# Optimization experiments

Hardware: AMD Instinct MI355X
Metric: run time of the kernel (lower is better)

Reference implementation:

```python
import jax, jax.numpy as jnp
import numpy as np

N_NODES = 40000
N_EDGES = 640000
IN_DIM, HID_DIM, OUT_DIM = 512, 128, 40


def setup_inputs() -> dict:
    key = jax.random.key(0)
    ks = jax.random.split(key, 8)
    x = jax.random.normal(ks[0], (N_NODES, IN_DIM), dtype=jnp.float32)
    edge_row = jax.random.randint(ks[1], (N_EDGES,), 0, N_NODES, dtype=jnp.int32)
    edge_col = jax.random.randint(ks[2], (N_EDGES,), 0, N_NODES, dtype=jnp.int32)
    edge_val = jax.random.uniform(ks[3], (N_EDGES,), dtype=jnp.float32)
    # Xavier-uniform init like nn.init.xavier_uniform_
    lim1 = float(np.sqrt(6.0 / (IN_DIM + HID_DIM)))
    lim2 = float(np.sqrt(6.0 / (HID_DIM + OUT_DIM)))
    W1 = jax.random.uniform(ks[4], (IN_DIM, HID_DIM), minval=-lim1, maxval=lim1, dtype=jnp.float32)
    W2 = jax.random.uniform(ks[5], (HID_DIM, OUT_DIM), minval=-lim2, maxval=lim2, dtype=jnp.float32)
    b1 = jnp.zeros((HID_DIM,), dtype=jnp.float32)
    b2 = jnp.zeros((OUT_DIM,), dtype=jnp.float32)
    return {"x": x, "edge_row": edge_row, "edge_col": edge_col, "edge_val": edge_val,
            "W1": W1, "b1": b1, "W2": W2, "b2": b2}


def _spmm(edge_row, edge_col, edge_val, y):
    # sparse adj @ y : gather source-node rows, scale by edge weight, scatter-add to dest
    msgs = edge_val[:, None] * y[edge_col]            # [E, d]
    return jax.ops.segment_sum(msgs, edge_row, num_segments=N_NODES)  # [N, d]


def reference(x, edge_row, edge_col, edge_val, W1, b1, W2, b2):
    # layer 1: dense projection + SpMM + bias
    h = _spmm(edge_row, edge_col, edge_val, x @ W1) + b1   # [N, hid]
    h = jax.nn.relu(h)
    # dropout is identity in eval mode (reference runs in eval)
    # layer 2
    o = _spmm(edge_row, edge_col, edge_val, h @ W2) + b2   # [N, out]
    return jax.nn.log_softmax(o, axis=1)
```

## Files before the change

kernel.cpp:

```cpp
#include <hip/hip_runtime.h>
#include <hip/hip_bf16.h>
#include <math.h>

#define N_NODES 40000
#define N_EDGES 640000
#define IN_DIM 512
#define HID_DIM 128
#define OUT_DIM 40
#define W2_PAD 48
#define SEG 64

typedef __attribute__((ext_vector_type(8))) short bf16x8_t;
typedef __attribute__((ext_vector_type(4))) float f32x4_t;

static __device__ __forceinline__ unsigned short f2bf(float f) {
    unsigned u = __float_as_uint(f);
    u += 0x7FFFu + ((u >> 16) & 1u);
    return (unsigned short)(u >> 16);
}
static __device__ __forceinline__ float bflo(unsigned g) { return __uint_as_float(g << 16); }
static __device__ __forceinline__ float bfhi(unsigned g) { return __uint_as_float(g & 0xFFFF0000u); }

__global__ __launch_bounds__(256) void convert_zero_kernel(const float* __restrict__ W1,
                                                           const float* __restrict__ W2,
                                                           unsigned short* __restrict__ w1t,
                                                           unsigned short* __restrict__ w2t,
                                                           int* __restrict__ cursor) {
    int idx = blockIdx.x * 256 + threadIdx.x;
    if (idx < N_NODES / 4) {
        reinterpret_cast<int4*>(cursor)[idx] = make_int4(0, 0, 0, 0);
    }
    if (idx < IN_DIM * HID_DIM) {
        int k = idx >> 7;
        int n = idx & 127;
        w1t[n * IN_DIM + k] = f2bf(W1[idx]);
    } else if (idx < IN_DIM * HID_DIM + W2_PAD * HID_DIM) {
        int j = idx - IN_DIM * HID_DIM;
        int n = j >> 7;
        int k = j & 127;
        w2t[n * HID_DIM + k] = (n < OUT_DIM) ? f2bf(W2[k * OUT_DIM + n]) : 0;
    }
}

__global__ __launch_bounds__(256) void scatter_kernel(const int* __restrict__ erow,
                                                      const int* __restrict__ ecol,
                                                      const float* __restrict__ eval,
                                                      int* __restrict__ cursor,
                                                      unsigned* __restrict__ sortedP) {
    int e = blockIdx.x * 256 + threadIdx.x;
    if (e < N_EDGES) {
        int r = erow[e];
        int pos = atomicAdd(&cursor[r], 1);
        sortedP[r * SEG + pos] = (unsigned)ecol[e] | ((unsigned)f2bf(eval[e]) << 16);
    }
}

__global__ __launch_bounds__(256) void gemm1_mfma_kernel(const float* __restrict__ x,
                                                         const unsigned short* __restrict__ w1t,
                                                         unsigned short* __restrict__ y1b) {
    __shared__ unsigned short Al[64][40];
    __shared__ unsigned short Bl[128][40];
    const int t    = threadIdx.x;
    const int wave = t >> 6;
    const int lane = t & 63;
    const int m0   = blockIdx.x * 64;
    const int mrow = lane & 15;
    const int quad = lane >> 4;

    const int ar = t >> 2;
    const int ac = (t & 3) * 8;
    const float* xptr = &x[(size_t)(m0 + ar) * IN_DIM + ac];
    const unsigned short* bptr0 = &w1t[(size_t)(t >> 2) * IN_DIM + (t & 3) * 8];
    const unsigned short* bptr1 = bptr0 + (size_t)64 * IN_DIM;

    f32x4_t acc[8];
#pragma unroll
    for (int i = 0; i < 8; ++i) acc[i] = (f32x4_t){0.f, 0.f, 0.f, 0.f};

    float4 xa = *reinterpret_cast<const float4*>(xptr);
    float4 xb = *reinterpret_cast<const float4*>(xptr + 4);
    int4   bw0 = *reinterpret_cast<const int4*>(bptr0);
    int4   bw1 = *reinterpret_cast<const int4*>(bptr1);

    for (int k0 = 0; k0 < IN_DIM; k0 += 32) {
        {
            union { int4 v; __hip_bfloat162 b[4]; } pk;
            pk.b[0] = __float22bfloat162_rn(make_float2(xa.x, xa.y));
            pk.b[1] = __float22bfloat162_rn(make_float2(xa.z, xa.w));
            pk.b[2] = __float22bfloat162_rn(make_float2(xb.x, xb.y));
            pk.b[3] = __float22bfloat162_rn(make_float2(xb.z, xb.w));
            *reinterpret_cast<int4*>(&Al[ar][ac]) = pk.v;
            *reinterpret_cast<int4*>(&Bl[t >> 2][(t & 3) * 8]) = bw0;
            *reinterpret_cast<int4*>(&Bl[64 + (t >> 2)][(t & 3) * 8]) = bw1;
        }
        __syncthreads();

        if (k0 + 32 < IN_DIM) {
            xa  = *reinterpret_cast<const float4*>(xptr + k0 + 32);
            xb  = *reinterpret_cast<const float4*>(xptr + k0 + 36);
            bw0 = *reinterpret_cast<const int4*>(bptr0 + k0 + 32);
            bw1 = *reinterpret_cast<const int4*>(bptr1 + k0 + 32);
        }

        bf16x8_t a = *reinterpret_cast<const bf16x8_t*>(&Al[wave * 16 + mrow][quad * 8]);
#pragma unroll
        for (int nt = 0; nt < 8; ++nt) {
            bf16x8_t b = *reinterpret_cast<const bf16x8_t*>(&Bl[nt * 16 + mrow][quad * 8]);
            acc[nt] = __builtin_amdgcn_mfma_f32_16x16x32_bf16(a, b, acc[nt], 0, 0, 0);
        }
        __syncthreads();
    }

#pragma unroll
    for (int nt = 0; nt < 8; ++nt) {
#pragma unroll
        for (int reg = 0; reg < 4; ++reg) {
            int row = m0 + wave * 16 + quad * 4 + reg;
            y1b[(size_t)row * HID_DIM + nt * 16 + mrow] = f2bf(acc[nt][reg]);
        }
    }
}

__global__ __launch_bounds__(256) void spmm1_kernel(const int* __restrict__ counts,
                                                    const unsigned* __restrict__ sortedP,
                                                    const unsigned short* __restrict__ y1b,
                                                    const float* __restrict__ b1,
                                                    unsigned short* __restrict__ h_bf) {
    const int lane = threadIdx.x & 63;
    const int q    = lane >> 4;
    const int fl   = lane & 15;
    const int row  = blockIdx.x * 4 + (threadIdx.x >> 6);
    const int cnt  = counts[row];
    unsigned meta  = (lane < cnt) ? sortedP[row * SEG + lane] : 0u;
    float a[8] = {0.f, 0.f, 0.f, 0.f, 0.f, 0.f, 0.f, 0.f};

    for (int j = 0; j < cnt; j += 8) {
        unsigned p0 = (unsigned)__shfl((int)meta, j + q, 64);
        unsigned p1 = (unsigned)__shfl((int)meta, j + 4 + q, 64);
        float v0 = __uint_as_float(p0 & 0xFFFF0000u);
        float v1 = __uint_as_float(p1 & 0xFFFF0000u);
        int   c0 = p0 & 0xFFFF;
        int   c1 = p1 & 0xFFFF;
        uint4 g0 = *reinterpret_cast<const uint4*>(&y1b[(size_t)c0 * HID_DIM + fl * 8]);
        uint4 g1 = *reinterpret_cast<const uint4*>(&y1b[(size_t)c1 * HID_DIM + fl * 8]);
        a[0] += v0 * bflo(g0.x); a[1] += v0 * bfhi(g0.x);
        a[2] += v0 * bflo(g0.y); a[3] += v0 * bfhi(g0.y);
        a[4] += v0 * bflo(g0.z); a[5] += v0 * bfhi(g0.z);
        a[6] += v0 * bflo(g0.w); a[7] += v0 * bfhi(g0.w);
        a[0] += v1 * bflo(g1.x); a[1] += v1 * bfhi(g1.x);
        a[2] += v1 * bflo(g1.y); a[3] += v1 * bfhi(g1.y);
        a[4] += v1 * bflo(g1.z); a[5] += v1 * bfhi(g1.z);
        a[6] += v1 * bflo(g1.w); a[7] += v1 * bfhi(g1.w);
    }
#pragma unroll
    for (int i = 0; i < 8; ++i) {
        a[i] += __shfl_xor(a[i], 16, 64);
        a[i] += __shfl_xor(a[i], 32, 64);
    }
    if (q == 0) {
        float4 vb0 = *reinterpret_cast<const float4*>(&b1[fl * 8]);
        float4 vb1 = *reinterpret_cast<const float4*>(&b1[fl * 8 + 4]);
        union { uint4 v; __hip_bfloat162 b[4]; } pk;
        pk.b[0] = __float22bfloat162_rn(make_float2(fmaxf(a[0] + vb0.x, 0.f), fmaxf(a[1] + vb0.y, 0.f)));
        pk.b[1] = __float22bfloat162_rn(make_float2(fmaxf(a[2] + vb0.z, 0.f), fmaxf(a[3] + vb0.w, 0.f)));
        pk.b[2] = __float22bfloat162_rn(make_float2(fmaxf(a[4] + vb1.x, 0.f), fmaxf(a[5] + vb1.y, 0.f)));
        pk.b[3] = __float22bfloat162_rn(make_float2(fmaxf(a[6] + vb1.z, 0.f), fmaxf(a[7] + vb1.w, 0.f)));
        *reinterpret_cast<uint4*>(&h_bf[(size_t)row * HID_DIM + fl * 8]) = pk.v;
    }
}

__global__ __launch_bounds__(256) void gemm2_mfma_kernel(const unsigned short* __restrict__ h_bf,
                                                         const unsigned short* __restrict__ w2t,
                                                         unsigned short* __restrict__ y2) {
    __shared__ unsigned short Hs[64][136];
    __shared__ unsigned short Ws[W2_PAD][136];
    const int t    = threadIdx.x;
    const int wave = t >> 6;
    const int lane = t & 63;
    const int m0   = blockIdx.x * 64;
    const int mrow = lane & 15;
    const int quad = lane >> 4;

#pragma unroll
    for (int i = 0; i < 4; ++i) {
        int flat = i * 256 + t;
        int r = flat >> 4;
        int c = (flat & 15) * 8;
        *reinterpret_cast<int4*>(&Hs[r][c]) =
            *reinterpret_cast<const int4*>(&h_bf[(size_t)(m0 + r) * HID_DIM + c]);
    }
#pragma unroll
    for (int i = 0; i < 3; ++i) {
        int flat = i * 256 + t;
        int n = flat >> 4;
        int c = (flat & 15) * 8;
        *reinterpret_cast<int4*>(&Ws[n][c]) =
            *reinterpret_cast<const int4*>(&w2t[(size_t)n * HID_DIM + c]);
    }
    __syncthreads();

    f32x4_t acc[3];
#pragma unroll
    for (int i = 0; i < 3; ++i) acc[i] = (f32x4_t){0.f, 0.f, 0.f, 0.f};
#pragma unroll
    for (int k0 = 0; k0 < HID_DIM; k0 += 32) {
        bf16x8_t a = *reinterpret_cast<const bf16x8_t*>(&Hs[wave * 16 + mrow][k0 + quad * 8]);
#pragma unroll
        for (int nt = 0; nt < 3; ++nt) {
            bf16x8_t b = *reinterpret_cast<const bf16x8_t*>(&Ws[nt * 16 + mrow][k0 + quad * 8]);
            acc[nt] = __builtin_amdgcn_mfma_f32_16x16x32_bf16(a, b, acc[nt], 0, 0, 0);
        }
    }
#pragma unroll
    for (int nt = 0; nt < 3; ++nt) {
        int col = nt * 16 + mrow;
        if (col < OUT_DIM) {
#pragma unroll
            for (int reg = 0; reg < 4; ++reg) {
                int row = m0 + wave * 16 + quad * 4 + reg;
                y2[(size_t)row * OUT_DIM + col] = f2bf(acc[nt][reg]);
            }
        }
    }
}

__global__ __launch_bounds__(256) void spmm2_lsm_kernel(const int* __restrict__ counts,
                                                        const unsigned* __restrict__ sortedP,
                                                        const unsigned short* __restrict__ y2,
                                                        const float* __restrict__ b2,
                                                        float* __restrict__ out) {
    const int lane = threadIdx.x & 63;
    const int q    = lane >> 4;
    const int fl   = lane & 15;
    const bool act = fl < 10;
    const int row  = blockIdx.x * 4 + (threadIdx.x >> 6);
    const int cnt  = counts[row];
    unsigned meta  = (lane < cnt) ? sortedP[row * SEG + lane] : 0u;
    float a[4] = {0.f, 0.f, 0.f, 0.f};

    for (int j = 0; j < cnt; j += 8) {
        unsigned p0 = (unsigned)__shfl((int)meta, j + q, 64);
        unsigned p1 = (unsigned)__shfl((int)meta, j + 4 + q, 64);
        if (act) {
            float v0 = __uint_as_float(p0 & 0xFFFF0000u);
            float v1 = __uint_as_float(p1 & 0xFFFF0000u);
            int   c0 = p0 & 0xFFFF;
            int   c1 = p1 & 0xFFFF;
            uint2 g0 = *reinterpret_cast<const uint2*>(&y2[(size_t)c0 * OUT_DIM + fl * 4]);
            uint2 g1 = *reinterpret_cast<const uint2*>(&y2[(size_t)c1 * OUT_DIM + fl * 4]);
            a[0] += v0 * bflo(g0.x); a[1] += v0 * bfhi(g0.x);
            a[2] += v0 * bflo(g0.y); a[3] += v0 * bfhi(g0.y);
            a[0] += v1 * bflo(g1.x); a[1] += v1 * bfhi(g1.x);
            a[2] += v1 * bflo(g1.y); a[3] += v1 * bfhi(g1.y);
        }
    }
#pragma unroll
    for (int i = 0; i < 4; ++i) {
        a[i] += __shfl_xor(a[i], 16, 64);
        a[i] += __shfl_xor(a[i], 32, 64);
    }
    float val[4];
    float ml = -INFINITY;
    if (act) {
        float4 vb = *reinterpret_cast<const float4*>(&b2[fl * 4]);
        val[0] = a[0] + vb.x; val[1] = a[1] + vb.y;
        val[2] = a[2] + vb.z; val[3] = a[3] + vb.w;
        ml = fmaxf(fmaxf(val[0], val[1]), fmaxf(val[2], val[3]));
    }
#pragma unroll
    for (int off = 1; off < 16; off <<= 1) ml = fmaxf(ml, __shfl_xor(ml, off, 64));
    float sl = 0.f;
    if (act) sl = expf(val[0] - ml) + expf(val[1] - ml) + expf(val[2] - ml) + expf(val[3] - ml);
#pragma unroll
    for (int off = 1; off < 16; off <<= 1) sl += __shfl_xor(sl, off, 64);
    if (act && q == 0) {
        float lg = logf(sl);
        float4 o = make_float4(val[0] - ml - lg, val[1] - ml - lg,
                               val[2] - ml - lg, val[3] - ml - lg);
        *reinterpret_cast<float4*>(&out[(size_t)row * OUT_DIM + fl * 4]) = o;
    }
}

extern "C" void kernel_launch(void* const* d_in, const int* in_sizes, int n_in,
                              void* d_out, int out_size, void* d_ws, size_t ws_size,
                              hipStream_t stream) {
    const float* x    = (const float*)d_in[0];
    const int*   erow = (const int*)d_in[1];
    const int*   ecol = (const int*)d_in[2];
    const float* eval = (const float*)d_in[3];
    const float* W1   = (const float*)d_in[4];
    const float* b1   = (const float*)d_in[5];
    const float* W2   = (const float*)d_in[6];
    const float* b2   = (const float*)d_in[7];
    float* out = (float*)d_out;

    char* p = (char*)d_ws;
    unsigned short* h_bf = (unsigned short*)p; p += (size_t)N_NODES * HID_DIM * 2;
    unsigned* sortedP = (unsigned*)p;          p += (size_t)N_NODES * SEG * 4;
    unsigned short* y1b = (unsigned short*)p;  p += (size_t)N_NODES * HID_DIM * 2;
    unsigned short* y2  = (unsigned short*)p;  p += (size_t)N_NODES * OUT_DIM * 2;
    int*   cursor    = (int*)p;                p += (size_t)N_NODES * 4;
    unsigned short* w1t = (unsigned short*)p;  p += (size_t)HID_DIM * IN_DIM * 2;
    unsigned short* w2t = (unsigned short*)p;

    convert_zero_kernel<<<(IN_DIM * HID_DIM + W2_PAD * HID_DIM + 255) / 256, 256, 0, stream>>>(
        W1, W2, w1t, w2t, cursor);
    scatter_kernel<<<(N_EDGES + 255) / 256, 256, 0, stream>>>(erow, ecol, eval, cursor, sortedP);

    gemm1_mfma_kernel<<<N_NODES / 64, 256, 0, stream>>>(x, w1t, y1b);
    spmm1_kernel<<<N_NODES / 4, 256, 0, stream>>>(cursor, sortedP, y1b, b1, h_bf);

    gemm2_mfma_kernel<<<N_NODES / 64, 256, 0, stream>>>(h_bf, w2t, y2);
    spmm2_lsm_kernel<<<N_NODES / 4, 256, 0, stream>>>(cursor, sortedP, y2, b2, out);
}
```

Before: 235.7 us.

## Fuse layer-1 SpMM with second projection and vectorize edge scatter

Measured after the change: 264.0 us. 12.0% more time.

```diff
diff --git a/kernel.cpp b/kernel.cpp
--- a/kernel.cpp
+++ b/kernel.cpp
@@ -20,6 +20,7 @@
 }
 static __device__ __forceinline__ float bflo(unsigned g) { return __uint_as_float(g << 16); }
 static __device__ __forceinline__ float bfhi(unsigned g) { return __uint_as_float(g & 0xFFFF0000u); }
+static __device__ __forceinline__ float bf1(unsigned short u) { return __uint_as_float(((unsigned)u) << 16); }
 
 __global__ __launch_bounds__(256) void convert_zero_kernel(const float* __restrict__ W1,
                                                            const float* __restrict__ W2,
@@ -47,11 +48,16 @@
                                                       const float* __restrict__ eval,
                                                       int* __restrict__ cursor,
                                                       unsigned* __restrict__ sortedP) {
-    int e = blockIdx.x * 256 + threadIdx.x;
-    if (e < N_EDGES) {
-        int r = erow[e];
-        int pos = atomicAdd(&cursor[r], 1);
-        sortedP[r * SEG + pos] = (unsigned)ecol[e] | ((unsigned)f2bf(eval[e]) << 16);
+    int i = blockIdx.x * 256 + threadIdx.x;
+    if (i < N_EDGES / 4) {
+        int4   r4 = reinterpret_cast<const int4*>(erow)[i];
+        int4   c4 = reinterpret_cast<const int4*>(ecol)[i];
+        float4 v4 = reinterpret_cast<const float4*>(eval)[i];
+        int p;
+        p = atomicAdd(&cursor[r4.x], 1); sortedP[r4.x * SEG + p] = (unsigned)c4.x | ((unsigned)f2bf(v4.x) << 16);
+        p = atomicAdd(&cursor[r4.y], 1); sortedP[r4.y * SEG + p] = (unsigned)c4.y | ((unsigned)f2bf(v4.y) << 16);
+        p = atomicAdd(&cursor[r4.z], 1); sortedP[r4.z * SEG + p] = (unsigned)c4.z | ((unsigned)f2bf(v4.z) << 16);
+        p = atomicAdd(&cursor[r4.w], 1); sortedP[r4.w * SEG + p] = (unsigned)c4.w | ((unsigned)f2bf(v4.w) << 16);
     }
 }
 
@@ -121,15 +127,18 @@
     }
 }
 
-__global__ __launch_bounds__(256) void spmm1_kernel(const int* __restrict__ counts,
-                                                    const unsigned* __restrict__ sortedP,
-                                                    const unsigned short* __restrict__ y1b,
-                                                    const float* __restrict__ b1,
-                                                    unsigned short* __restrict__ h_bf) {
+__global__ __launch_bounds__(256) void spmm1_gemm2_kernel(const int* __restrict__ counts,
+                                                          const unsigned* __restrict__ sortedP,
+                                                          const unsigned short* __restrict__ y1b,
+                                                          const float* __restrict__ b1,
+                                                          const unsigned short* __restrict__ w2t,
+                                                          unsigned short* __restrict__ y2) {
+    __shared__ float hs[4][HID_DIM];
     const int lane = threadIdx.x & 63;
     const int q    = lane >> 4;
     const int fl   = lane & 15;
-    const int row  = blockIdx.x * 4 + (threadIdx.x >> 6);
+    const int wave = threadIdx.x >> 6;
+    const int row  = blockIdx.x * 4 + wave;
     const int cnt  = counts[row];
     unsigned meta  = (lane < cnt) ? sortedP[row * SEG + lane] : 0u;
     float a[8] = {0.f, 0.f, 0.f, 0.f, 0.f, 0.f, 0.f, 0.f};
@@ -160,67 +169,38 @@
     if (q == 0) {
         float4 vb0 = *reinterpret_cast<const float4*>(&b1[fl * 8]);
         float4 vb1 = *reinterpret_cast<const float4*>(&b1[fl * 8 + 4]);
-        union { uint4 v; __hip_bfloat162 b[4]; } pk;
-        pk.b[0] = __float22bfloat162_rn(make_float2(fmaxf(a[0] + vb0.x, 0.f), fmaxf(a[1] + vb0.y, 0.f)));
-        pk.b[1] = __float22bfloat162_rn(make_float2(fmaxf(a[2] + vb0.z, 0.f), fmaxf(a[3] + vb0.w, 0.f)));
-        pk.b[2] = __float22bfloat162_rn(make_float2(fmaxf(a[4] + vb1.x, 0.f), fmaxf(a[5] + vb1.y, 0.f)));
-        pk.b[3] = __float22bfloat162_rn(make_float2(fmaxf(a[6] + vb1.z, 0.f), fmaxf(a[7] + vb1.w, 0.f)));
-        *reinterpret_cast<uint4*>(&h_bf[(size_t)row * HID_DIM + fl * 8]) = pk.v;
-    }
-}
-
-__global__ __launch_bounds__(256) void gemm2_mfma_kernel(const unsigned short* __restrict__ h_bf,
-                                                         const unsigned short* __restrict__ w2t,
-                                                         unsigned short* __restrict__ y2) {
-    __shared__ unsigned short Hs[64][136];
-    __shared__ unsigned short Ws[W2_PAD][136];
-    const int t    = threadIdx.x;
-    const int wave = t >> 6;
-    const int lane = t & 63;
-    const int m0   = blockIdx.x * 64;
-    const int mrow = lane & 15;
-    const int quad = lane >> 4;
-
-#pragma unroll
-    for (int i = 0; i < 4; ++i) {
-        int flat = i * 256 + t;
-        int r = flat >> 4;
-        int c = (flat & 15) * 8;
-        *reinterpret_cast<int4*>(&Hs[r][c]) =
-            *reinterpret_cast<const int4*>(&h_bf[(size_t)(m0 + r) * HID_DIM + c]);
-    }
-#pragma unroll
-    for (int i = 0; i < 3; ++i) {
-        int flat = i * 256 + t;
-        int n = flat >> 4;
-        int c = (flat & 15) * 8;
-        *reinterpret_cast<int4*>(&Ws[n][c]) =
-            *reinterpret_cast<const int4*>(&w2t[(size_t)n * HID_DIM + c]);
+        float hb[8];
+        hb[0] = bf1(f2bf(fmaxf(a[0] + vb0.x, 0.f)));
+        hb[1] = bf1(f2bf(fmaxf(a[1] + vb0.y, 0.f)));
+        hb[2] = bf1(f2bf(fmaxf(a[2] + vb0.z, 0.f)));
+        hb[3] = bf1(f2bf(fmaxf(a[3] + vb0.w, 0.f)));
+        hb[4] = bf1(f2bf(fmaxf(a[4] + vb1.x, 0.f)));
+        hb[5] = bf1(f2bf(fmaxf(a[5] + vb1.y, 0.f)));
+        hb[6] = bf1(f2bf(fmaxf(a[6] + vb1.z, 0.f)));
+        hb[7] = bf1(f2bf(fmaxf(a[7] + vb1.w, 0.f)));
+        *reinterpret_cast<float4*>(&hs[wave][fl * 8])     = make_float4(hb[0], hb[1], hb[2], hb[3]);
+        *reinterpret_cast<float4*>(&hs[wave][fl * 8 + 4]) = make_float4(hb[4], hb[5], hb[6], hb[7]);
     }
     __syncthreads();
 
-    f32x4_t acc[3];
-#pragma unroll
-    for (int i = 0; i < 3; ++i) acc[i] = (f32x4_t){0.f, 0.f, 0.f, 0.f};
-#pragma unroll
-    for (int k0 = 0; k0 < HID_DIM; k0 += 32) {
-        bf16x8_t a = *reinterpret_cast<const bf16x8_t*>(&Hs[wave * 16 + mrow][k0 + quad * 8]);
-#pragma unroll
-        for (int nt = 0; nt < 3; ++nt) {
-            bf16x8_t b = *reinterpret_cast<const bf16x8_t*>(&Ws[nt * 16 + mrow][k0 + quad * 8]);
-            acc[nt] = __builtin_amdgcn_mfma_f32_16x16x32_bf16(a, b, acc[nt], 0, 0, 0);
-        }
-    }
-#pragma unroll
-    for (int nt = 0; nt < 3; ++nt) {
-        int col = nt * 16 + mrow;
-        if (col < OUT_DIM) {
-#pragma unroll
-            for (int reg = 0; reg < 4; ++reg) {
-                int row = m0 + wave * 16 + quad * 4 + reg;
-                y2[(size_t)row * OUT_DIM + col] = f2bf(acc[nt][reg]);
-            }
-        }
+    if (lane < OUT_DIM) {
+        const unsigned short* wrow = &w2t[(size_t)lane * HID_DIM];
+        float y = 0.f;
+#pragma unroll
+        for (int k0 = 0; k0 < HID_DIM; k0 += 8) {
+            bf16x8_t w8 = *reinterpret_cast<const bf16x8_t*>(wrow + k0);
+            float4 h0 = *reinterpret_cast<const float4*>(&hs[wave][k0]);
+            float4 h1 = *reinterpret_cast<const float4*>(&hs[wave][k0 + 4]);
+            y += h0.x * bf1((unsigned short)w8[0]);
+            y += h0.y * bf1((unsigned short)w8[1]);
+            y += h0.z * bf1((unsigned short)w8[2]);
+            y += h0.w * bf1((unsigned short)w8[3]);
+            y += h1.x * bf1((unsigned short)w8[4]);
+            y += h1.y * bf1((unsigned short)w8[5]);
+            y += h1.z * bf1((unsigned short)w8[6]);
+            y += h1.w * bf1((unsigned short)w8[7]);
+        }
+        y2[(size_t)row * OUT_DIM + lane] = f2bf(y);
     }
 }
 
@@ -295,7 +275,6 @@
     float* out = (float*)d_out;
 
     char* p = (char*)d_ws;
-    unsigned short* h_bf = (unsigned short*)p; p += (size_t)N_NODES * HID_DIM * 2;
     unsigned* sortedP = (unsigned*)p;          p += (size_t)N_NODES * SEG * 4;
     unsigned short* y1b = (unsigned short*)p;  p += (size_t)N_NODES * HID_DIM * 2;
     unsigned short* y2  = (unsigned short*)p;  p += (size_t)N_NODES * OUT_DIM * 2;
@@ -305,11 +284,9 @@
 
     convert_zero_kernel<<<(IN_DIM * HID_DIM + W2_PAD * HID_DIM + 255) / 256, 256, 0, stream>>>(
         W1, W2, w1t, w2t, cursor);
-    scatter_kernel<<<(N_EDGES + 255) / 256, 256, 0, stream>>>(erow, ecol, eval, cursor, sortedP);
+    scatter_kernel<<<(N_EDGES / 4 + 255) / 256, 256, 0, stream>>>(erow, ecol, eval, cursor, sortedP);
 
     gemm1_mfma_kernel<<<N_NODES / 64, 256, 0, stream>>>(x, w1t, y1b);
-    spmm1_kernel<<<N_NODES / 4, 256, 0, stream>>>(cursor, sortedP, y1b, b1, h_bf);
-
-    gemm2_mfma_kernel<<<N_NODES / 64, 256, 0, stream>>>(h_bf, w2t, y2);
+    spmm1_gemm2_kernel<<<N_NODES / 4, 256, 0, stream>>>(cursor, sortedP, y1b, b1, w2t, y2);
     spmm2_lsm_kernel<<<N_NODES / 4, 256, 0, stream>>>(cursor, sortedP, y2, b2, out);
 }
```
